# Kernel tuning notes

Measured on AMD Instinct MI355X. Metric: run time of the kernel, lower is better.

## Reference

```python
import jax, jax.numpy as jnp
import numpy as np

B, L, DK, DV = 16, 8192, 128, 128
ALPHA, LR, BETA = 0.02, 0.1, 0.9
SCALE = 0.05  # keeps lr*||k||^2 small -> stable delta-rule recurrence


def setup_inputs() -> dict:
    key = jax.random.key(0)
    kq, kk, kv = jax.random.split(key, 3)
    Q = jax.random.normal(kq, (B, L, DK), dtype=jnp.float32) * SCALE
    K = jax.random.normal(kk, (B, L, DK), dtype=jnp.float32) * SCALE
    V = jax.random.normal(kv, (B, L, DV), dtype=jnp.float32) * SCALE
    return {"Q": Q, "K": K, "V": V}


def reference(Q, K, V):
    # TitansMemory: reset -> per-step update_step(k_t, v_t) -> read(q_t).
    # W_t = (1-alpha) W_{t-1} - lr * m_t,  m_t = beta m_{t-1} + (1-beta) grad_t
    # grad_t = 2 (W_{t-1} k_t - v_t) k_t^T ;  y_t = W_t q_t
    b, l, dk = K.shape
    dv = V.shape[-1]
    W0 = jnp.zeros((b, dv, dk), dtype=K.dtype)
    m0 = jnp.zeros_like(W0)

    def step(carry, inp):
        W, m = carry
        k, v, q = inp  # [B,dk], [B,dv], [B,dk]
        resid = jnp.einsum('bvk,bk->bv', W, k) - v          # Wk - v
        grad = 2.0 * resid[:, :, None] * k[:, None, :]       # [B,dv,dk]
        m = BETA * m + (1.0 - BETA) * grad
        W = (1.0 - ALPHA) * W - LR * m
        y = jnp.einsum('bvk,bk->bv', W, q)                   # read with updated W
        return (W, m), y

    xs = (jnp.swapaxes(K, 0, 1), jnp.swapaxes(V, 0, 1), jnp.swapaxes(Q, 0, 1))
    (_, _), Y = jax.lax.scan(step, (W0, m0), xs)             # Y: [L,B,dv]
    return jnp.swapaxes(Y, 0, 1)                              # [B,L,dv]
```

## Files before the change

kernel.cpp:

```cpp
#include <hip/hip_runtime.h>


#define L_ 8192
#define D_ 128

typedef __attribute__((ext_vector_type(4))) float f4;
typedef __attribute__((ext_vector_type(2))) float f2;
typedef __attribute__((ext_vector_type(2))) unsigned int u2;

constexpr float A_    = 0.98f;
constexpr float BETA_ = 0.9f;
constexpr float C_S   = -0.02f;
constexpr float CA_   = C_S * A_;
constexpr float CB_   = C_S * BETA_;
constexpr float CV_   = -C_S;

template <int CTRL>
__device__ __forceinline__ float dpp_add(float x) {
  int y = __builtin_amdgcn_update_dpp(0, __float_as_int(x), CTRL, 0xF, 0xF, true);
  return x + __int_as_float(y);
}

__device__ __forceinline__ float fold4(f4 d) {
  f2 t = {d.x + d.z, d.y + d.w};
  return t.x + t.y;
}

__device__ __forceinline__ u2 swap16(float a, float b) {
  return __builtin_amdgcn_permlane16_swap(__float_as_uint(a), __float_as_uint(b),
                                          false, false);
}

__device__ __forceinline__ f2 reduce2(float a, float b) {
  u2 r = swap16(a, b);
  float c = __uint_as_float(r.x) + __uint_as_float(r.y);
  c = dpp_add<0x121>(c);
  c = dpp_add<0x122>(c);
  c = dpp_add<0x124>(c);
  c = dpp_add<0x128>(c);
  u2 u = swap16(c, c);
  return {__uint_as_float(u.x),
          __uint_as_float(u.y)};
}

#define GLD4(dst, addr, OFF) \
  asm volatile("global_load_dwordx4 %0, %1, off offset:" OFF : "=v"(dst) : "v"(addr))
#define GLD1(dst, addr, OFF) \
  asm volatile("global_load_dword %0, %1, off offset:" OFF : "=v"(dst) : "v"(addr))

#define ISSUE_CHUNK(kb, qb, vb)                            \
  do {                                                     \
    GLD4(kb[0], ka64, "0");    GLD4(qb[0], qa64, "0");    GLD1(vb[0], va64, "0");    \
    GLD4(kb[1], ka64, "512");  GLD4(qb[1], qa64, "512");  GLD1(vb[1], va64, "512");  \
    GLD4(kb[2], ka64, "1024"); GLD4(qb[2], qa64, "1024"); GLD1(vb[2], va64, "1024"); \
    GLD4(kb[3], ka64, "1536"); GLD4(qb[3], qa64, "1536"); GLD1(vb[3], va64, "1536"); \
    GLD4(kb[4], ka64, "2048"); GLD4(qb[4], qa64, "2048"); GLD1(vb[4], va64, "2048"); \
    GLD4(kb[5], ka64, "2560"); GLD4(qb[5], qa64, "2560"); GLD1(vb[5], va64, "2560"); \
    GLD4(kb[6], ka64, "3072"); GLD4(qb[6], qa64, "3072"); GLD1(vb[6], va64, "3072"); \
    GLD4(kb[7], ka64, "3584"); GLD4(qb[7], qa64, "3584"); GLD1(vb[7], va64, "3584"); \
    uint64_t bump_ = (sc < 1023) ? 4096u : 0u;             \
    ka64 += bump_; qa64 += bump_; va64 += bump_; ++sc;     \
  } while (0)

#define WAITP                                              \
  do {                                                     \
    asm volatile("s_waitcnt vmcnt(24)");                   \
    __builtin_amdgcn_sched_barrier(0);                     \
  } while (0)

__global__ __launch_bounds__(64, 1)
void TitansMemory_188978561365_kernel(const float* __restrict__ Q,
                                      const float* __restrict__ K,
                                      const float* __restrict__ V,
                                      float* __restrict__ Y) {
  const int lane  = threadIdx.x;
  const int wid   = blockIdx.x;
  const int batch = wid >> 6;
  const int col   = (lane & 31) << 2;

  const size_t bbase = (size_t)batch * (size_t)L_ * D_;
  uint64_t ka64 = (uint64_t)(K + bbase + col);
  uint64_t qa64 = (uint64_t)(Q + bbase + col);
  uint64_t va64 = (uint64_t)(V + bbase + ((wid & 63) << 1) + (lane >> 5));
  float* yb = Y + bbase + ((wid & 63) << 1) + (lane >> 5)
                + (size_t)((lane >> 4) & 1) * D_;
  int sc = 0;

  const f4 av = {A_, A_, A_, A_};
  const f4 bv = {BETA_, BETA_, BETA_, BETA_};

  f4 w = {0.f, 0.f, 0.f, 0.f}, m = {0.f, 0.f, 0.f, 0.f};
  float ey[8];

  f4 kA[8], qA[8]; float vA[8];
  f4 kB[8], qB[8]; float vB[8];

  auto apply = [&](float s, const f4& kj, const f4& qj, float& eyj) {
    f4 s4 = {s, s, s, s};
    m = __builtin_elementwise_fma(s4, kj, bv * m);
    w = __builtin_elementwise_fma(av, w, m);
    eyj = fold4(w * qj);
  };

  auto mkbase = [&](const f4& kp2, float vp2) -> float {
    f2 P = reduce2(fold4(w * kp2), fold4(m * kp2));
    return fmaf(CA_, P.x, fmaf(CB_, P.y, CV_ * vp2));
  };

  auto window = [&](f4 (&kX)[8], f4 (&qX)[8], float (&vX)[8]) {
    f2 h0  = reduce2(fold4(w * kX[0]), fold4(w * kX[1]));
    f2 h1  = reduce2(fold4(m * kX[1]), fold4(kX[0] * kX[1]));
    f2 g23 = reduce2(fold4(kX[1] * kX[2]), fold4(kX[2] * kX[3]));
    f2 g45 = reduce2(fold4(kX[3] * kX[4]), fold4(kX[4] * kX[5]));
    f2 g67 = reduce2(fold4(kX[5] * kX[6]), fold4(kX[6] * kX[7]));

    float s = fmaf(C_S, h0.x, CV_ * vX[0]);
    apply(s, kX[0], qX[0], ey[0]);
    float b2 = mkbase(kX[2], vX[2]);
    float base1 = fmaf(CA_, h0.y, fmaf(CB_, h1.x, CV_ * vX[1]));
    s = fmaf(s, C_S * h1.y, base1);
    apply(s, kX[1], qX[1], ey[1]);
    float b3 = mkbase(kX[3], vX[3]);
    s = fmaf(s, C_S * g23.x, b2);
    apply(s, kX[2], qX[2], ey[2]);
    float b4 = mkbase(kX[4], vX[4]);
    s = fmaf(s, C_S * g23.y, b3);
    apply(s, kX[3], qX[3], ey[3]);
    float b5 = mkbase(kX[5], vX[5]);
    s = fmaf(s, C_S * g45.x, b4);
    apply(s, kX[4], qX[4], ey[4]);
    float b6 = mkbase(kX[6], vX[6]);
    s = fmaf(s, C_S * g45.y, b5);
    apply(s, kX[5], qX[5], ey[5]);
    float b7 = mkbase(kX[7], vX[7]);
    s = fmaf(s, C_S * g67.x, b6);
    apply(s, kX[6], qX[6], ey[6]);
    s = fmaf(s, C_S * g67.y, b7);
    apply(s, kX[7], qX[7], ey[7]);

#pragma unroll
    for (int p = 0; p < 4; ++p) {
      u2 r = swap16(ey[2 * p], ey[2 * p + 1]);
      float c = __uint_as_float(r.x) + __uint_as_float(r.y);
      c = dpp_add<0x121>(c);
      c = dpp_add<0x122>(c);
      c = dpp_add<0x124>(c);
      c = dpp_add<0x128>(c);
      if ((lane & 15) == 0) yb[(size_t)(2 * p) * D_] = c;
    }
    yb += 8 * D_;
    ISSUE_CHUNK(kX, qX, vX);
  };

  ISSUE_CHUNK(kA, qA, vA);
  ISSUE_CHUNK(kB, qB, vB);

  for (int it = 0; it < 512; ++it) {
    WAITP;
    window(kA, qA, vA);
    WAITP;
    window(kB, qB, vB);
  }
}

extern "C" void kernel_launch(void* const* d_in, const int* in_sizes, int n_in,
                              void* d_out, int out_size, void* d_ws, size_t ws_size,
                              hipStream_t stream) {
  const float* Q = (const float*)d_in[0];
  const float* K = (const float*)d_in[1];
  const float* V = (const float*)d_in[2];
  float* Y = (float*)d_out;
  dim3 grid(1024), block(64);
  hipLaunchKernelGGL(TitansMemory_188978561365_kernel, grid, block, 0, stream,
                     Q, K, V, Y);
}
```

Measured before the change: 1.294 ms.

## Restructure delta-rule recurrence into 4-step blocked solve with Gram precompute

Replaces the per-step sequential scalar recurrence, which needed one cross-lane reduction per step to extend the residual, with 4-step sub-windows. Each sub-window starts from the current W/m state combined with precomputed decay coefficients, and uses a small triangular solve over a 6-entry Gram matrix of the chunk's keys. This takes the per-step reductions off the serial dependency chain and batches them, so reduction latency can overlap. The cost is more vector FMAs per sub-window and possibly different floating-point rounding.

```diff
diff --git a/kernel.cpp b/kernel.cpp
--- a/kernel.cpp
+++ b/kernel.cpp
@@ -11,9 +11,20 @@
 constexpr float A_    = 0.98f;
 constexpr float BETA_ = 0.9f;
 constexpr float C_S   = -0.02f;
-constexpr float CA_   = C_S * A_;
-constexpr float CB_   = C_S * BETA_;
 constexpr float CV_   = -C_S;
+
+constexpr float PH1_  = A_ + BETA_;
+constexpr float PH2_  = A_ * A_ + A_ * BETA_ + BETA_ * BETA_;
+constexpr float T0_   = C_S;
+constexpr float T1_   = C_S * PH1_;
+constexpr float T2_   = C_S * PH2_;
+constexpr float CSA0_ = C_S;
+constexpr float CSA1_ = C_S * A_;
+constexpr float CSA2_ = C_S * A_ * A_;
+constexpr float CSA3_ = C_S * A_ * A_ * A_;
+constexpr float CSC1_ = C_S * BETA_;
+constexpr float CSC2_ = C_S * BETA_ * PH1_;
+constexpr float CSC3_ = C_S * BETA_ * PH2_;
 
 template <int CTRL>
 __device__ __forceinline__ float dpp_add(float x) {
@@ -39,8 +50,7 @@
   c = dpp_add<0x124>(c);
   c = dpp_add<0x128>(c);
   u2 u = swap16(c, c);
-  return {__uint_as_float(u.x),
-          __uint_as_float(u.y)};
+  return {__uint_as_float(u.x), __uint_as_float(u.y)};
 }
 
 #define GLD4(dst, addr, OFF) \
@@ -68,6 +78,29 @@
     __builtin_amdgcn_sched_barrier(0);                     \
   } while (0)
 
+#define SUBWIN(kX, qX, vX, O, G)                                         \
+  do {                                                                   \
+    f4 u0 = vcsa0 * w;                                                   \
+    f4 u1 = __builtin_elementwise_fma(vcsa1, w, vcsc1 * m);              \
+    f4 u2 = __builtin_elementwise_fma(vcsa2, w, vcsc2 * m);              \
+    f4 u3 = __builtin_elementwise_fma(vcsa3, w, vcsc3 * m);              \
+    f2 d01 = reduce2(fold4(u0 * kX[O + 0]), fold4(u1 * kX[O + 1]));      \
+    f2 d23 = reduce2(fold4(u2 * kX[O + 2]), fold4(u3 * kX[O + 3]));      \
+    float b0 = fmaf(CV_, vX[O + 0], d01.x);                              \
+    float b1 = fmaf(CV_, vX[O + 1], d01.y);                              \
+    float b2 = fmaf(CV_, vX[O + 2], d23.x);                              \
+    float b3 = fmaf(CV_, vX[O + 3], d23.y);                              \
+    float s0 = b0;                                                       \
+    float s1 = fmaf(T0_ * G[0], s0, b1);                                 \
+    float s2 = fmaf(T0_ * G[3], s1, fmaf(T1_ * G[1], s0, b2));           \
+    float s3 = fmaf(T0_ * G[5], s2,                                      \
+                fmaf(T1_ * G[4], s1, fmaf(T2_ * G[2], s0, b3)));         \
+    apply(s0, kX[O + 0], qX[O + 0], ey[O + 0]);                          \
+    apply(s1, kX[O + 1], qX[O + 1], ey[O + 1]);                          \
+    apply(s2, kX[O + 2], qX[O + 2], ey[O + 2]);                          \
+    apply(s3, kX[O + 3], qX[O + 3], ey[O + 3]);                          \
+  } while (0)
+
 __global__ __launch_bounds__(64, 1)
 void TitansMemory_188978561365_kernel(const float* __restrict__ Q,
                                       const float* __restrict__ K,
@@ -88,6 +121,13 @@
 
   const f4 av = {A_, A_, A_, A_};
   const f4 bv = {BETA_, BETA_, BETA_, BETA_};
+  const f4 vcsa0 = {CSA0_, CSA0_, CSA0_, CSA0_};
+  const f4 vcsa1 = {CSA1_, CSA1_, CSA1_, CSA1_};
+  const f4 vcsa2 = {CSA2_, CSA2_, CSA2_, CSA2_};
+  const f4 vcsa3 = {CSA3_, CSA3_, CSA3_, CSA3_};
+  const f4 vcsc1 = {CSC1_, CSC1_, CSC1_, CSC1_};
+  const f4 vcsc2 = {CSC2_, CSC2_, CSC2_, CSC2_};
+  const f4 vcsc3 = {CSC3_, CSC3_, CSC3_, CSC3_};
 
   f4 w = {0.f, 0.f, 0.f, 0.f}, m = {0.f, 0.f, 0.f, 0.f};
   float ey[8];
@@ -102,42 +142,22 @@
     eyj = fold4(w * qj);
   };
 
-  auto mkbase = [&](const f4& kp2, float vp2) -> float {
-    f2 P = reduce2(fold4(w * kp2), fold4(m * kp2));
-    return fmaf(CA_, P.x, fmaf(CB_, P.y, CV_ * vp2));
-  };
-
-  auto window = [&](f4 (&kX)[8], f4 (&qX)[8], float (&vX)[8]) {
-    f2 h0  = reduce2(fold4(w * kX[0]), fold4(w * kX[1]));
-    f2 h1  = reduce2(fold4(m * kX[1]), fold4(kX[0] * kX[1]));
-    f2 g23 = reduce2(fold4(kX[1] * kX[2]), fold4(kX[2] * kX[3]));
-    f2 g45 = reduce2(fold4(kX[3] * kX[4]), fold4(kX[4] * kX[5]));
-    f2 g67 = reduce2(fold4(kX[5] * kX[6]), fold4(kX[6] * kX[7]));
-
-    float s = fmaf(C_S, h0.x, CV_ * vX[0]);
-    apply(s, kX[0], qX[0], ey[0]);
-    float b2 = mkbase(kX[2], vX[2]);
-    float base1 = fmaf(CA_, h0.y, fmaf(CB_, h1.x, CV_ * vX[1]));
-    s = fmaf(s, C_S * h1.y, base1);
-    apply(s, kX[1], qX[1], ey[1]);
-    float b3 = mkbase(kX[3], vX[3]);
-    s = fmaf(s, C_S * g23.x, b2);
-    apply(s, kX[2], qX[2], ey[2]);
-    float b4 = mkbase(kX[4], vX[4]);
-    s = fmaf(s, C_S * g23.y, b3);
-    apply(s, kX[3], qX[3], ey[3]);
-    float b5 = mkbase(kX[5], vX[5]);
-    s = fmaf(s, C_S * g45.x, b4);
-    apply(s, kX[4], qX[4], ey[4]);
-    float b6 = mkbase(kX[6], vX[6]);
-    s = fmaf(s, C_S * g45.y, b5);
-    apply(s, kX[5], qX[5], ey[5]);
-    float b7 = mkbase(kX[7], vX[7]);
-    s = fmaf(s, C_S * g67.x, b6);
-    apply(s, kX[6], qX[6], ey[6]);
-    s = fmaf(s, C_S * g67.y, b7);
-    apply(s, kX[7], qX[7], ey[7]);
-
+  auto chunk = [&](f4 (&kX)[8], f4 (&qX)[8], float (&vX)[8]) {
+    float Ga[6], Gb[6];
+    {
+      f2 gA = reduce2(fold4(kX[0] * kX[1]), fold4(kX[0] * kX[2]));
+      f2 gB = reduce2(fold4(kX[0] * kX[3]), fold4(kX[1] * kX[2]));
+      f2 gC = reduce2(fold4(kX[1] * kX[3]), fold4(kX[2] * kX[3]));
+      Ga[0] = gA.x; Ga[1] = gA.y; Ga[2] = gB.x;
+      Ga[3] = gB.y; Ga[4] = gC.x; Ga[5] = gC.y;
+      f2 gD = reduce2(fold4(kX[4] * kX[5]), fold4(kX[4] * kX[6]));
+      f2 gE = reduce2(fold4(kX[4] * kX[7]), fold4(kX[5] * kX[6]));
+      f2 gF = reduce2(fold4(kX[5] * kX[7]), fold4(kX[6] * kX[7]));
+      Gb[0] = gD.x; Gb[1] = gD.y; Gb[2] = gE.x;
+      Gb[3] = gE.y; Gb[4] = gF.x; Gb[5] = gF.y;
+    }
+    SUBWIN(kX, qX, vX, 0, Ga);
+    SUBWIN(kX, qX, vX, 4, Gb);
 #pragma unroll
     for (int p = 0; p < 4; ++p) {
       u2 r = swap16(ey[2 * p], ey[2 * p + 1]);
@@ -157,9 +177,9 @@
 
   for (int it = 0; it < 512; ++it) {
     WAITP;
-    window(kA, qA, vA);
+    chunk(kA, qA, vA);
     WAITP;
-    window(kB, qB, vB);
+    chunk(kB, qB, vB);
   }
 }
 
```

New measurement: 1.343 ms. 3.8% more time.
